# Optimization experiments

Hardware: AMD Instinct MI355X
Metric: run time of the kernel (lower is better)

The kernel has to match this reference:

```python
import jax, jax.numpy as jnp
import numpy as np

NUM_CLASSES = 256
N_ITERS = 25  # fixed Lloyd iterations (sklearn default max_iter=300; fixed count for a jit-able reference)


def setup_inputs() -> dict:
    key = jax.random.key(0)
    k1, k2 = jax.random.split(key)
    features = jax.random.normal(k1, (65536, 1024), dtype=jnp.float32)
    logits = jax.random.normal(k2, (65536, 256), dtype=jnp.float32)
    return {"features": features, "logits": logits}


def _segment_mean_centroids(features, labels, num_classes, prev_centroids):
    # scatter-mean of features into per-class centroids; keep previous centroid if a class is empty
    sums = jax.ops.segment_sum(features, labels, num_segments=num_classes)      # [C, D]
    counts = jax.ops.segment_sum(jnp.ones((features.shape[0],), features.dtype),
                                 labels, num_segments=num_classes)               # [C]
    has = counts > 0
    means = sums / jnp.maximum(counts, 1.0)[:, None]
    return jnp.where(has[:, None], means, prev_centroids)


def _assign(features, centroids):
    # argmin of squared euclidean distance; ||x||^2 term is constant per row, drop it
    # scores[n, c] = -2 x_n . mu_c + ||mu_c||^2
    scores = -2.0 * jnp.einsum('nd,cd->nc', features, centroids) + jnp.sum(centroids * centroids, axis=1)[None, :]
    return jnp.argmin(scores, axis=1)


def reference(features, logits):
    # KMeans.forward: labels = argmax(logits); centroids init from label centers (centroid_init='label_centers');
    # then Lloyd's k-means (sklearn KMeans with init=centroids, n_init=1) and return cluster labels.
    init_labels = jnp.argmax(logits, axis=1)
    # get_centroids: empty classes stay at zero
    zeros = jnp.zeros((NUM_CLASSES, features.shape[1]), features.dtype)
    centroids = _segment_mean_centroids(features, init_labels, NUM_CLASSES, zeros)

    def body(i, centroids):
        labels = _assign(features, centroids)
        return _segment_mean_centroids(features, labels, NUM_CLASSES, centroids)

    centroids = jax.lax.fori_loop(0, N_ITERS, body, centroids)
    pseudo_labels = _assign(features, centroids)
    return pseudo_labels.astype(jnp.int64)
```

## Files before the change

### kernel.cpp

```cpp
#include <hip/hip_runtime.h>

#define N_PTS 65536
#define DIM   1024
#define NCLS  256
#define NITER 25

typedef __attribute__((ext_vector_type(8)))  short short8;
typedef __attribute__((ext_vector_type(16))) float f32x16;

__device__ __forceinline__ unsigned short bf_split(float x, float& rem) {
    unsigned u = __float_as_uint(x);
    unsigned b = (u + 0x7fffu + ((u >> 16) & 1u)) & 0xffff0000u;
    rem = x - __uint_as_float(b);
    return (unsigned short)(b >> 16);
}
__device__ __forceinline__ unsigned short bf_rne(float x) {
    unsigned u = __float_as_uint(x);
    return (unsigned short)((u + 0x7fffu + ((u >> 16) & 1u)) >> 16);
}

__device__ __forceinline__ void gload_lds16(const void* g, void* l) {
    __builtin_amdgcn_global_load_lds(
        (const __attribute__((address_space(1))) unsigned int*)g,
        (__attribute__((address_space(3))) unsigned int*)l, 16, 0, 0);
}

__global__ void k_argmax(const float* __restrict__ logits, int* __restrict__ labels) {
    int row  = blockIdx.x * 4 + (threadIdx.x >> 6);
    int lane = threadIdx.x & 63;
    float4 v = reinterpret_cast<const float4*>(logits + (size_t)row * NCLS)[lane];
    float bv = v.x; int bi = lane * 4;
    if (v.y > bv) { bv = v.y; bi = lane * 4 + 1; }
    if (v.z > bv) { bv = v.z; bi = lane * 4 + 2; }
    if (v.w > bv) { bv = v.w; bi = lane * 4 + 3; }
    #pragma unroll
    for (int off = 32; off >= 1; off >>= 1) {
        float ov = __shfl_down(bv, off, 64);
        int   oi = __shfl_down(bi, off, 64);
        if (ov > bv || (ov == bv && oi < bi)) { bv = ov; bi = oi; }
    }
    if (lane == 0) labels[row] = bi;
}

__global__ void k_hist(const int* __restrict__ labels, int* __restrict__ counts) {
    __shared__ int h[NCLS];
    h[threadIdx.x] = 0;
    __syncthreads();
    for (int i = blockIdx.x * blockDim.x + threadIdx.x; i < N_PTS;
         i += gridDim.x * blockDim.x)
        atomicAdd(&h[labels[i]], 1);
    __syncthreads();
    int v = h[threadIdx.x];
    if (v) atomicAdd(&counts[threadIdx.x], v);
}

__global__ __launch_bounds__(512) void k_accum(const float* __restrict__ feat,
                                               const int* __restrict__ labels,
                                               float* __restrict__ partials) {
    __shared__ unsigned long long s[NCLS * 32];
    int tid = threadIdx.x;
    for (int i = tid; i < NCLS * 32; i += 512) s[i] = 0ull;
    __syncthreads();
    int slice = blockIdx.x;
    int chunk = blockIdx.y;
    int w = tid >> 6, l = tid & 63;
    int sub = l >> 3;
    int dq  = l & 7;
    const size_t dbase = (size_t)slice * 32 + dq * 4;
    for (int step = 0; step < 128; ++step) {
        int p = chunk * 8192 + step * 64 + w * 8 + sub;
        int c = labels[p];
        float4 f = *reinterpret_cast<const float4*>(feat + (size_t)p * DIM + dbase);
        unsigned long long* dst = &s[c * 32 + dq * 4];
        atomicAdd(dst + 0, (unsigned long long)__double2ll_rn((double)f.x * 16777216.0));
        atomicAdd(dst + 1, (unsigned long long)__double2ll_rn((double)f.y * 16777216.0));
        atomicAdd(dst + 2, (unsigned long long)__double2ll_rn((double)f.z * 16777216.0));
        atomicAdd(dst + 3, (unsigned long long)__double2ll_rn((double)f.w * 16777216.0));
    }
    __syncthreads();
    float* out = partials + (size_t)chunk * NCLS * DIM;
    for (int i = tid; i < NCLS * 32; i += 512) {
        int c = i >> 5, d = i & 31;
        out[(size_t)c * DIM + slice * 32 + d] =
            (float)((double)(long long)s[i] * (1.0 / 16777216.0));
    }
}

__global__ void k_finalize(const float* __restrict__ partials,
                           const int* __restrict__ counts,
                           float* __restrict__ centroids) {
    int idx = blockIdx.x * blockDim.x + threadIdx.x;
    int c = idx >> 8;
    size_t off = (size_t)idx * 4;
    float4 sum = make_float4(0.f, 0.f, 0.f, 0.f);
    for (int ch = 0; ch < 8; ++ch) {
        float4 p = *reinterpret_cast<const float4*>(partials + (size_t)ch * NCLS * DIM + off);
        sum.x += p.x; sum.y += p.y; sum.z += p.z; sum.w += p.w;
    }
    int cnt = counts[c];
    float4 outv;
    if (cnt > 0) {
        float fc = (float)cnt;
        outv = make_float4(sum.x / fc, sum.y / fc, sum.z / fc, sum.w / fc);
    } else {
        outv = *reinterpret_cast<const float4*>(centroids + off);
    }
    *reinterpret_cast<float4*>(centroids + off) = outv;
}

__global__ void k_norms(const float* __restrict__ centroids, float* __restrict__ norms) {
    int c = blockIdx.x;
    int t = threadIdx.x;
    float4 v = reinterpret_cast<const float4*>(centroids + (size_t)c * DIM)[t];
    float s = v.x * v.x + v.y * v.y + v.z * v.z + v.w * v.w;
    __shared__ float red[4];
    #pragma unroll
    for (int off = 32; off >= 1; off >>= 1) s += __shfl_down(s, off, 64);
    if ((t & 63) == 0) red[t >> 6] = s;
    __syncthreads();
    if (t == 0) norms[c] = red[0] + red[1] + red[2] + red[3];
}

__global__ void k_splitB(const float* __restrict__ cent, unsigned short* __restrict__ Bs) {
    int lin = blockIdx.x * 256 + threadIdx.x;
    int n = lin & 255, kg = lin >> 8;
    int k = kg * 8;
    int kc = kg >> 2, kh = (kg >> 1) & 1, jg = kg & 1;
    int nt = n >> 5, lane = (n & 31) + 32 * jg;
    const float* src = cent + (size_t)n * DIM + k;
    unsigned short hi[8], mi[8], lo[8];
    #pragma unroll
    for (int j = 0; j < 8; ++j) {
        float r1, r2;
        hi[j] = bf_split(src[j], r1);
        mi[j] = bf_split(r1, r2);
        lo[j] = bf_rne(r2);
    }
    #pragma unroll
    for (int p = 0; p < 3; ++p) {
        size_t base = ((((size_t)kc * 3 + p) * 8 + nt) * 2 + kh) * 512 + (size_t)lane * 8;
        const unsigned short* srcp = (p == 0) ? hi : (p == 1) ? mi : lo;
        uint4 pack = *reinterpret_cast<const uint4*>(srcp);
        *reinterpret_cast<uint4*>(Bs + base) = pack;
    }
}

__global__ __launch_bounds__(256, 2) void k_assign(
        const float* __restrict__ feat, const unsigned short* __restrict__ Bs,
        const float* __restrict__ norms, int* __restrict__ out_labels) {
    __shared__ __align__(16) unsigned short Bl[48 * 512];
    int tid = threadIdx.x, w = tid >> 6, l = tid & 63;
    int cn = l & 31, jg = l >> 5;
    int p0 = blockIdx.x * 128;

    f32x16 acc[8];
    #pragma unroll
    for (int t = 0; t < 8; ++t)
        #pragma unroll
        for (int i = 0; i < 16; ++i) acc[t][i] = 0.f;

    const float* arow = feat + (size_t)(p0 + w * 32 + cn) * DIM + jg * 8;

    for (int kc = 0; kc < 32; ++kc) {
        int k0 = kc * 32;
        float4 g0 = *reinterpret_cast<const float4*>(arow + k0);
        float4 g1 = *reinterpret_cast<const float4*>(arow + k0 + 4);
        float4 g2 = *reinterpret_cast<const float4*>(arow + k0 + 16);
        float4 g3 = *reinterpret_cast<const float4*>(arow + k0 + 20);
        __syncthreads();
        #pragma unroll
        for (int i = 0; i < 12; ++i) {
            int s = w * 12 + i;
            int kh = s & 1, ntl = (s >> 1) & 7, q = s >> 4;
            const unsigned short* g =
                Bs + ((((size_t)kc * 3 + q) * 8 + ntl) * 2 + kh) * 512 + (size_t)l * 8;
            gload_lds16(g, &Bl[s * 512]);
        }
        float xs[16] = {g0.x, g0.y, g0.z, g0.w, g1.x, g1.y, g1.z, g1.w,
                        g2.x, g2.y, g2.z, g2.w, g3.x, g3.y, g3.z, g3.w};
        union { short8 v; unsigned short u[8]; } af[2][3];
        #pragma unroll
        for (int kh = 0; kh < 2; ++kh)
            #pragma unroll
            for (int j = 0; j < 8; ++j) {
                float r1, r2;
                af[kh][0].u[j] = bf_split(xs[kh * 8 + j], r1);
                af[kh][1].u[j] = bf_split(r1, r2);
                af[kh][2].u[j] = bf_rne(r2);
            }
        __syncthreads();
        #pragma unroll
        for (int q = 0; q < 3; ++q)
            #pragma unroll
            for (int kh = 0; kh < 2; ++kh) {
                short8 bf[8];
                #pragma unroll
                for (int ntl = 0; ntl < 8; ++ntl)
                    bf[ntl] = *reinterpret_cast<const short8*>(
                        &Bl[((q * 8 + ntl) * 2 + kh) * 512 + l * 8]);
                const int np = (q == 0) ? 3 : (q == 1) ? 2 : 1;
                #pragma unroll
                for (int p = 0; p < 3; ++p) {
                    if (p < np) {
                        #pragma unroll
                        for (int ntl = 0; ntl < 8; ++ntl)
                            acc[ntl] = __builtin_amdgcn_mfma_f32_32x32x16_bf16(
                                af[kh][p].v, bf[ntl], acc[ntl], 0, 0, 0);
                    }
                }
            }
    }

    float nrm[8];
    #pragma unroll
    for (int ntl = 0; ntl < 8; ++ntl) nrm[ntl] = norms[ntl * 32 + cn];
    #pragma unroll
    for (int r = 0; r < 16; ++r) {
        unsigned long long key = ~0ull;
        #pragma unroll
        for (int ntl = 0; ntl < 8; ++ntl) {
            float s = nrm[ntl] - 2.0f * acc[ntl][r];
            unsigned u = __float_as_uint(s);
            u = (u & 0x80000000u) ? ~u : (u | 0x80000000u);
            unsigned long long kk =
                ((unsigned long long)u << 32) | (unsigned)(ntl * 32 + cn);
            key = (kk < key) ? kk : key;
        }
        #pragma unroll
        for (int off = 16; off >= 1; off >>= 1) {
            unsigned long long ok = __shfl_xor(key, off, 64);
            key = (ok < key) ? ok : key;
        }
        if (cn == 0) {
            int m = p0 + w * 32 + (r & 3) + 8 * (r >> 2) + 4 * jg;
            out_labels[m] = (int)(key & 0xffffffffull);
        }
    }
}

extern "C" void kernel_launch(void* const* d_in, const int* in_sizes, int n_in,
                              void* d_out, int out_size, void* d_ws, size_t ws_size,
                              hipStream_t stream) {
    const float* feat   = (const float*)d_in[0];
    const float* logits = (const float*)d_in[1];
    int* out_labels = (int*)d_out;

    char* ws = (char*)d_ws;
    float* centroids            = (float*)ws;
    float* partials             = (float*)(ws + 0x100000);
    float* norms                = (float*)(ws + 0x900000);
    int*   counts               = (int*)  (ws + 0x901000);
    int*   labels               = (int*)  (ws + 0x902000);
    unsigned short* Bs          = (unsigned short*)(ws + 0x950000);

    k_argmax<<<N_PTS / 4, 256, 0, stream>>>(logits, labels);
    hipMemsetAsync(centroids, 0, (size_t)NCLS * DIM * sizeof(float), stream);
    hipMemsetAsync(counts, 0, NCLS * sizeof(int), stream);
    k_hist<<<64, 256, 0, stream>>>(labels, counts);
    k_accum<<<dim3(32, 8), 512, 0, stream>>>(feat, labels, partials);
    k_finalize<<<256, 256, 0, stream>>>(partials, counts, centroids);

    for (int it = 0; it < NITER; ++it) {
        k_norms<<<NCLS, 256, 0, stream>>>(centroids, norms);
        k_splitB<<<128, 256, 0, stream>>>(centroids, Bs);
        k_assign<<<N_PTS / 128, 256, 0, stream>>>(feat, Bs, norms, labels);
        hipMemsetAsync(counts, 0, NCLS * sizeof(int), stream);
        k_hist<<<64, 256, 0, stream>>>(labels, counts);
        k_accum<<<dim3(32, 8), 512, 0, stream>>>(feat, labels, partials);
        k_finalize<<<256, 256, 0, stream>>>(partials, counts, centroids);
    }

    k_norms<<<NCLS, 256, 0, stream>>>(centroids, norms);
    k_splitB<<<128, 256, 0, stream>>>(centroids, Bs);
    k_assign<<<N_PTS / 128, 256, 0, stream>>>(feat, Bs, norms, out_labels);
}
```

Baseline: 7.016 ms.

## Pipeline assign GEMM over B precision phases and fuse norms, split, histogram

The assign kernel now streams each k-chunk's B operand in three smaller LDS buffers, one per precision level. Loads of the next level and next A chunk overlap the MFMAs on the current level, using manual waitcnt, barriers and setprio. Norms and bf16 splitting of the centroids move into the finalize kernel, and the label histogram moves into the assign epilogue through shared-memory atomics. This removes three launches per iteration and hides global load latency, at the cost of fragile hand-written vmcnt accounting.

```diff
diff --git a/kernel.cpp b/kernel.cpp
--- a/kernel.cpp
+++ b/kernel.cpp
@@ -86,12 +86,13 @@
     }
 }
 
-__global__ void k_finalize(const float* __restrict__ partials,
-                           const int* __restrict__ counts,
-                           float* __restrict__ centroids) {
-    int idx = blockIdx.x * blockDim.x + threadIdx.x;
-    int c = idx >> 8;
-    size_t off = (size_t)idx * 4;
+__global__ void k_final(const float* __restrict__ partials,
+                        const int* __restrict__ counts,
+                        float* __restrict__ centroids,
+                        float* __restrict__ norms,
+                        unsigned short* __restrict__ Bs) {
+    int c = blockIdx.x, t = threadIdx.x;
+    size_t off = ((size_t)c * 256 + t) * 4;
     float4 sum = make_float4(0.f, 0.f, 0.f, 0.f);
     for (int ch = 0; ch < 8; ++ch) {
         float4 p = *reinterpret_cast<const float4*>(partials + (size_t)ch * NCLS * DIM + off);
@@ -106,52 +107,45 @@
         outv = *reinterpret_cast<const float4*>(centroids + off);
     }
     *reinterpret_cast<float4*>(centroids + off) = outv;
-}
-
-__global__ void k_norms(const float* __restrict__ centroids, float* __restrict__ norms) {
-    int c = blockIdx.x;
-    int t = threadIdx.x;
-    float4 v = reinterpret_cast<const float4*>(centroids + (size_t)c * DIM)[t];
-    float s = v.x * v.x + v.y * v.y + v.z * v.z + v.w * v.w;
+
+    float s = outv.x * outv.x + outv.y * outv.y + outv.z * outv.z + outv.w * outv.w;
     __shared__ float red[4];
     #pragma unroll
-    for (int off = 32; off >= 1; off >>= 1) s += __shfl_down(s, off, 64);
+    for (int o = 32; o >= 1; o >>= 1) s += __shfl_down(s, o, 64);
     if ((t & 63) == 0) red[t >> 6] = s;
     __syncthreads();
     if (t == 0) norms[c] = red[0] + red[1] + red[2] + red[3];
-}
-
-__global__ void k_splitB(const float* __restrict__ cent, unsigned short* __restrict__ Bs) {
-    int lin = blockIdx.x * 256 + threadIdx.x;
-    int n = lin & 255, kg = lin >> 8;
-    int k = kg * 8;
-    int kc = kg >> 2, kh = (kg >> 1) & 1, jg = kg & 1;
-    int nt = n >> 5, lane = (n & 31) + 32 * jg;
-    const float* src = cent + (size_t)n * DIM + k;
-    unsigned short hi[8], mi[8], lo[8];
-    #pragma unroll
-    for (int j = 0; j < 8; ++j) {
+
+    int k = t * 4;
+    int kc = k >> 5, kh = (k >> 4) & 1, jg = (k >> 3) & 1, j0 = k & 7;
+    int nt = c >> 5, lane = (c & 31) + 32 * jg;
+    float xv[4] = {outv.x, outv.y, outv.z, outv.w};
+    unsigned short hv[4], mv[4], lv[4];
+    #pragma unroll
+    for (int e = 0; e < 4; ++e) {
         float r1, r2;
-        hi[j] = bf_split(src[j], r1);
-        mi[j] = bf_split(r1, r2);
-        lo[j] = bf_rne(r2);
+        hv[e] = bf_split(xv[e], r1);
+        mv[e] = bf_split(r1, r2);
+        lv[e] = bf_rne(r2);
     }
     #pragma unroll
     for (int p = 0; p < 3; ++p) {
-        size_t base = ((((size_t)kc * 3 + p) * 8 + nt) * 2 + kh) * 512 + (size_t)lane * 8;
-        const unsigned short* srcp = (p == 0) ? hi : (p == 1) ? mi : lo;
-        uint4 pack = *reinterpret_cast<const uint4*>(srcp);
-        *reinterpret_cast<uint4*>(Bs + base) = pack;
+        size_t base = ((((size_t)kc * 3 + p) * 8 + nt) * 2 + kh) * 512 + (size_t)lane * 8 + j0;
+        const unsigned short* sp = (p == 0) ? hv : (p == 1) ? mv : lv;
+        *reinterpret_cast<uint2*>(&Bs[base]) = *reinterpret_cast<const uint2*>(sp);
     }
 }
 
 __global__ __launch_bounds__(256, 2) void k_assign(
         const float* __restrict__ feat, const unsigned short* __restrict__ Bs,
-        const float* __restrict__ norms, int* __restrict__ out_labels) {
-    __shared__ __align__(16) unsigned short Bl[48 * 512];
+        const float* __restrict__ norms, int* __restrict__ counts,
+        int* __restrict__ out_labels) {
+    __shared__ __align__(16) unsigned short Bl[3 * 16 * 512];
+    __shared__ int h[NCLS];
     int tid = threadIdx.x, w = tid >> 6, l = tid & 63;
     int cn = l & 31, jg = l >> 5;
     int p0 = blockIdx.x * 128;
+    h[tid] = 0;
 
     f32x16 acc[8];
     #pragma unroll
@@ -161,24 +155,29 @@
 
     const float* arow = feat + (size_t)(p0 + w * 32 + cn) * DIM + jg * 8;
 
-    for (int kc = 0; kc < 32; ++kc) {
-        int k0 = kc * 32;
-        float4 g0 = *reinterpret_cast<const float4*>(arow + k0);
-        float4 g1 = *reinterpret_cast<const float4*>(arow + k0 + 4);
-        float4 g2 = *reinterpret_cast<const float4*>(arow + k0 + 16);
-        float4 g3 = *reinterpret_cast<const float4*>(arow + k0 + 20);
-        __syncthreads();
-        #pragma unroll
-        for (int i = 0; i < 12; ++i) {
-            int s = w * 12 + i;
-            int kh = s & 1, ntl = (s >> 1) & 7, q = s >> 4;
-            const unsigned short* g =
-                Bs + ((((size_t)kc * 3 + q) * 8 + ntl) * 2 + kh) * 512 + (size_t)l * 8;
-            gload_lds16(g, &Bl[s * 512]);
-        }
-        float xs[16] = {g0.x, g0.y, g0.z, g0.w, g1.x, g1.y, g1.z, g1.w,
-                        g2.x, g2.y, g2.z, g2.w, g3.x, g3.y, g3.z, g3.w};
-        union { short8 v; unsigned short u[8]; } af[2][3];
+    union AF { short8 v; unsigned short u[8]; } af[2][3];
+    float4 ga0, ga1, ga2, ga3;
+
+    auto issue_b = [&](int kc_, int q_, int rb_) {
+        #pragma unroll
+        for (int i = 0; i < 4; ++i) {
+            int s = w * 4 + i;
+            const unsigned short* g = Bs +
+                ((((size_t)kc_ * 3 + q_) * 8 + (s >> 1)) * 2 + (s & 1)) * 512 +
+                (size_t)l * 8;
+            gload_lds16(g, &Bl[(rb_ * 16 + s) * 512]);
+        }
+    };
+    auto load_a = [&](int kc_) {
+        const float* ab = arow + kc_ * 32;
+        asm volatile("global_load_dwordx4 %0, %1, off"           : "=v"(ga0) : "v"(ab) : "memory");
+        asm volatile("global_load_dwordx4 %0, %1, off offset:16" : "=v"(ga1) : "v"(ab) : "memory");
+        asm volatile("global_load_dwordx4 %0, %1, off offset:64" : "=v"(ga2) : "v"(ab) : "memory");
+        asm volatile("global_load_dwordx4 %0, %1, off offset:80" : "=v"(ga3) : "v"(ab) : "memory");
+    };
+    auto split_a = [&]() {
+        float xs[16] = {ga0.x, ga0.y, ga0.z, ga0.w, ga1.x, ga1.y, ga1.z, ga1.w,
+                        ga2.x, ga2.y, ga2.z, ga2.w, ga3.x, ga3.y, ga3.z, ga3.w};
         #pragma unroll
         for (int kh = 0; kh < 2; ++kh)
             #pragma unroll
@@ -188,27 +187,62 @@
                 af[kh][1].u[j] = bf_split(r1, r2);
                 af[kh][2].u[j] = bf_rne(r2);
             }
-        __syncthreads();
-        #pragma unroll
-        for (int q = 0; q < 3; ++q)
+    };
+    auto mfma_phase = [&](int rb, int np) {
+        #pragma unroll
+        for (int kh = 0; kh < 2; ++kh) {
+            short8 bf[8];
             #pragma unroll
-            for (int kh = 0; kh < 2; ++kh) {
-                short8 bf[8];
-                #pragma unroll
-                for (int ntl = 0; ntl < 8; ++ntl)
-                    bf[ntl] = *reinterpret_cast<const short8*>(
-                        &Bl[((q * 8 + ntl) * 2 + kh) * 512 + l * 8]);
-                const int np = (q == 0) ? 3 : (q == 1) ? 2 : 1;
-                #pragma unroll
-                for (int p = 0; p < 3; ++p) {
-                    if (p < np) {
-                        #pragma unroll
-                        for (int ntl = 0; ntl < 8; ++ntl)
-                            acc[ntl] = __builtin_amdgcn_mfma_f32_32x32x16_bf16(
-                                af[kh][p].v, bf[ntl], acc[ntl], 0, 0, 0);
-                    }
+            for (int ntl = 0; ntl < 8; ++ntl)
+                bf[ntl] = *reinterpret_cast<const short8*>(
+                    &Bl[(rb * 16 + ntl * 2 + kh) * 512 + l * 8]);
+            #pragma unroll
+            for (int p = 0; p < 3; ++p)
+                if (p < np) {
+                    #pragma unroll
+                    for (int ntl = 0; ntl < 8; ++ntl)
+                        acc[ntl] = __builtin_amdgcn_mfma_f32_32x32x16_bf16(
+                            af[kh][p].v, bf[ntl], acc[ntl], 0, 0, 0);
                 }
-            }
+        }
+    };
+
+    issue_b(0, 0, 0);
+    load_a(0);
+    issue_b(0, 1, 1);
+    asm volatile("s_waitcnt vmcnt(4)" ::: "memory");
+    __builtin_amdgcn_sched_barrier(0);
+    split_a();
+
+    for (int kc = 0; kc < 32; ++kc) {
+        const bool lastk = (kc == 31);
+        asm volatile("s_waitcnt vmcnt(4)" ::: "memory");
+        __builtin_amdgcn_s_barrier();
+        issue_b(kc, 2, 2);
+        __builtin_amdgcn_s_setprio(1);
+        mfma_phase(0, 3);
+        __builtin_amdgcn_s_setprio(0);
+        asm volatile("s_waitcnt vmcnt(4)" ::: "memory");
+        __builtin_amdgcn_s_barrier();
+        if (!lastk) {
+            issue_b(kc + 1, 0, 0);
+            load_a(kc + 1);
+        }
+        __builtin_amdgcn_s_setprio(1);
+        mfma_phase(1, 2);
+        __builtin_amdgcn_s_setprio(0);
+        if (!lastk) { asm volatile("s_waitcnt vmcnt(8)" ::: "memory"); }
+        else        { asm volatile("s_waitcnt vmcnt(0)" ::: "memory"); }
+        __builtin_amdgcn_s_barrier();
+        if (!lastk) {
+            issue_b(kc + 1, 1, 1);
+            asm volatile("s_waitcnt vmcnt(4)" ::: "memory");
+            __builtin_amdgcn_sched_barrier(0);
+        }
+        __builtin_amdgcn_s_setprio(1);
+        mfma_phase(2, 1);
+        __builtin_amdgcn_s_setprio(0);
+        if (!lastk) split_a();
     }
 
     float nrm[8];
@@ -233,9 +267,14 @@
         }
         if (cn == 0) {
             int m = p0 + w * 32 + (r & 3) + 8 * (r >> 2) + 4 * jg;
-            out_labels[m] = (int)(key & 0xffffffffull);
-        }
-    }
+            int lab = (int)(key & 0xffffffffull);
+            out_labels[m] = lab;
+            atomicAdd(&h[lab], 1);
+        }
+    }
+    __syncthreads();
+    int v = h[tid];
+    if (v) atomicAdd(&counts[tid], v);
 }
 
 extern "C" void kernel_launch(void* const* d_in, const int* in_sizes, int n_in,
@@ -258,19 +297,14 @@
     hipMemsetAsync(counts, 0, NCLS * sizeof(int), stream);
     k_hist<<<64, 256, 0, stream>>>(labels, counts);
     k_accum<<<dim3(32, 8), 512, 0, stream>>>(feat, labels, partials);
-    k_finalize<<<256, 256, 0, stream>>>(partials, counts, centroids);
+    k_final<<<NCLS, 256, 0, stream>>>(partials, counts, centroids, norms, Bs);
 
     for (int it = 0; it < NITER; ++it) {
-        k_norms<<<NCLS, 256, 0, stream>>>(centroids, norms);
-        k_splitB<<<128, 256, 0, stream>>>(centroids, Bs);
-        k_assign<<<N_PTS / 128, 256, 0, stream>>>(feat, Bs, norms, labels);
         hipMemsetAsync(counts, 0, NCLS * sizeof(int), stream);
-        k_hist<<<64, 256, 0, stream>>>(labels, counts);
+        k_assign<<<N_PTS / 128, 256, 0, stream>>>(feat, Bs, norms, counts, labels);
         k_accum<<<dim3(32, 8), 512, 0, stream>>>(feat, labels, partials);
-        k_finalize<<<256, 256, 0, stream>>>(partials, counts, centroids);
-    }
-
-    k_norms<<<NCLS, 256, 0, stream>>>(centroids, norms);
-    k_splitB<<<128, 256, 0, stream>>>(centroids, Bs);
-    k_assign<<<N_PTS / 128, 256, 0, stream>>>(feat, Bs, norms, out_labels);
-}
+        k_final<<<NCLS, 256, 0, stream>>>(partials, counts, centroids, norms, Bs);
+    }
+
+    k_assign<<<N_PTS / 128, 256, 0, stream>>>(feat, Bs, norms, counts, out_labels);
+}
```

New measurement: 7.269 ms. 3.6% more time.
